# Optimization experiments

Hardware: AMD Instinct MI355X
Metric: run time of the kernel (lower is better)

## Reference

```python
import jax, jax.numpy as jnp
import numpy as np

DMIN, DMAX = -1.0, 1.0
B, I, O, K = 1024, 256, 256, 128

def setup_inputs() -> dict:
    key = jax.random.key(0)
    k1, k2, k3 = jax.random.split(key, 3)
    x = jax.random.normal(k1, (B, I), dtype=jnp.float32)
    bound = 1.0 / np.sqrt(I)
    base_weight = jax.random.uniform(k2, (O, I), dtype=jnp.float32, minval=-bound, maxval=bound)
    coeff = 0.03 * jax.random.normal(k3, (O, I, K), dtype=jnp.float32)
    coeff = coeff - coeff.mean(axis=-1, keepdims=True)
    return {
        'x': x,
        'base_weight': base_weight,
        'spline_coefficients': coeff,
        'spline_scale': jnp.ones((O, I), dtype=jnp.float32),
        'bias': jnp.zeros((O,), dtype=jnp.float32),
    }


def reference(x, base_weight, spline_coefficients, spline_scale, bias):
    num_knots = spline_coefficients.shape[-1]
    step = (DMAX - DMIN) / (num_knots - 1)
    # input activation (tanh) then clamp to spline domain
    p = jnp.tanh(x)                                   # (B, I)
    c = jnp.clip(p, DMIN, DMAX)
    scaled = (c - DMIN) / step                        # in [0, K-1]
    left = jnp.clip(jnp.floor(scaled).astype(jnp.int32), 0, num_knots - 1)
    right = jnp.minimum(left + 1, num_knots - 1)
    frac = scaled - left.astype(p.dtype)              # (B, I)
    # fold spline_scale into coefficients, then gather only the 2 relevant knots
    Cs = spline_coefficients * spline_scale[..., None]  # (O, I, K)
    ii = jnp.arange(x.shape[1])[None, :]                # (1, I) broadcasts with (B, I)
    cl = Cs[:, ii, left]                                # (O, B, I)
    cr = Cs[:, ii, right]                               # (O, B, I)
    spline = jnp.einsum('bi,obi->bo', 1.0 - frac, cl) + jnp.einsum('bi,obi->bo', frac, cr)
    base = jax.nn.silu(p) @ base_weight.T               # (B, O)
    return base + spline + bias[None, :]
```

## Files before the change

### kernel.cpp

```cpp
#include <hip/hip_runtime.h>

constexpr int Bb = 1024;
constexpr int Ii = 256;
constexpr int Oo = 256;
constexpr int Kk = 128;
constexpr int NCH = 8;

typedef unsigned short u16;
typedef u16 ushort4v __attribute__((ext_vector_type(4)));

__device__ __forceinline__ float bf16u_to_f(u16 u) {
    union { unsigned int ui; float f; } c;
    c.ui = ((unsigned int)u) << 16;
    return c.f;
}
__device__ __forceinline__ u16 f_to_bf16(float f) {
    union { float f; unsigned int u; } c; c.f = f;
    unsigned int r = c.u + 0x7fffu + ((c.u >> 16) & 1u);
    return (u16)(r >> 16);
}

__global__ __launch_bounds__(256) void kperm(const float* __restrict__ cs,
                                             const float* __restrict__ scale,
                                             const float* __restrict__ wbase,
                                             u16* __restrict__ cp,
                                             float* __restrict__ wt) {
    __shared__ u16 T[128 * 130];
    int i  = blockIdx.x >> 1;
    int o0 = (blockIdx.x & 1) << 7;
    int t = threadIdx.x;

    {
        int c4 = t & 31;
        int rb = t >> 5;
        const float4* cs4 = (const float4*)cs;
#pragma unroll
        for (int p = 0; p < 16; ++p) {
            int r = p * 8 + rb;
            int o = o0 + r;
            float sc = scale[o * Ii + i];
            float4 val = cs4[(size_t)(o * Ii + i) * (Kk / 4) + c4];
            unsigned int lo = ((unsigned int)f_to_bf16(val.y * sc) << 16) | f_to_bf16(val.x * sc);
            unsigned int hi = ((unsigned int)f_to_bf16(val.w * sc) << 16) | f_to_bf16(val.z * sc);
            *(unsigned int*)&T[r * 130 + c4 * 4]     = lo;
            *(unsigned int*)&T[r * 130 + c4 * 4 + 2] = hi;
        }
    }
    __syncthreads();
    {
        int ol = t & 127;
        int kh = t >> 7;
        u16* dst = cp + ((size_t)i * Kk) * Oo + o0 + ol;
#pragma unroll
        for (int p = 0; p < 64; ++p) {
            int k = p * 2 + kh;
            dst[(size_t)k * Oo] = T[ol * 130 + k];
        }
    }
    if (blockIdx.x < 256) {
        int gid = blockIdx.x * 256 + t;
        wt[gid] = wbase[(gid & 255) * Ii + (gid >> 8)];
    }
}

__global__ __launch_bounds__(256, 4) void kmain(const float* __restrict__ x,
                                                const char* __restrict__ cpb,
                                                const float4* __restrict__ wt4,
                                                float4* __restrict__ part4) {
    __shared__ float4 sf[128];
    int t = threadIdx.x;
    int blk = blockIdx.x;
    int chunk = blk & (NCH - 1);
    int b0 = (blk >> 3) << 2;
    int i0 = chunk << 5;

    if (t < 128) {
        int il = t >> 2, bl = t & 3;
        float xv = x[(size_t)(b0 + bl) * Ii + i0 + il];
        float e2 = __expf(2.f * xv);
        float p = 1.f - 2.f / (e2 + 1.f);
        float s = p / (1.f + __expf(-p));
        float c = fminf(fmaxf(p, -1.f), 1.f);
        float scaled = (c + 1.f) * ((float)(Kk - 1) * 0.5f);
        int l = (int)floorf(scaled);
        l = min(max(l, 0), Kk - 1);
        int rr = min(l + 1, Kk - 1);
        float4 v;
        v.x = scaled - (float)l;
        v.y = s;
        v.z = __int_as_float(l * (Oo * 2));
        v.w = __int_as_float(rr * (Oo * 2));
        sf[t] = v;
    }
    __syncthreads();

    int oq = t & 63;
    int bh = t >> 6;

    float a0 = 0.f, a1 = 0.f, a2 = 0.f, a3 = 0.f;
    const char* cbase = cpb + (size_t)i0 * (Kk * Oo * 2) + oq * 8;
#pragma unroll 8
    for (int il = 0; il < 32; ++il) {
        float4 v = sf[il * 4 + bh];
        float4 w = wt4[(i0 + il) * (Oo / 4) + oq];
        const char* ci = cbase + (size_t)il * (Kk * Oo * 2);
        ushort4v cl = *(const ushort4v*)(ci + __float_as_int(v.z));
        ushort4v cr = *(const ushort4v*)(ci + __float_as_int(v.w));
        float f = v.x, g = 1.f - v.x, s = v.y;
        a0 = fmaf(s, w.x, a0);
        a1 = fmaf(s, w.y, a1);
        a2 = fmaf(s, w.z, a2);
        a3 = fmaf(s, w.w, a3);
        a0 = fmaf(g, bf16u_to_f(cl.x), a0);
        a1 = fmaf(g, bf16u_to_f(cl.y), a1);
        a2 = fmaf(g, bf16u_to_f(cl.z), a2);
        a3 = fmaf(g, bf16u_to_f(cl.w), a3);
        a0 = fmaf(f, bf16u_to_f(cr.x), a0);
        a1 = fmaf(f, bf16u_to_f(cr.y), a1);
        a2 = fmaf(f, bf16u_to_f(cr.z), a2);
        a3 = fmaf(f, bf16u_to_f(cr.w), a3);
    }
    float4 r; r.x = a0; r.y = a1; r.z = a2; r.w = a3;
    part4[(size_t)chunk * (Bb * Oo / 4) + (size_t)(b0 + bh) * (Oo / 4) + oq] = r;
}

__global__ __launch_bounds__(256) void kreduce(const float4* __restrict__ part4,
                                               const float4* __restrict__ bias4,
                                               float4* __restrict__ out4) {
    int gid = blockIdx.x * 256 + threadIdx.x;
    const float4* p = part4 + gid;
    float4 s = p[0];
#pragma unroll
    for (int c = 1; c < NCH; ++c) {
        float4 v = p[(size_t)c * (Bb * Oo / 4)];
        s.x += v.x; s.y += v.y; s.z += v.z; s.w += v.w;
    }
    float4 bv = bias4[gid & 63];
    s.x += bv.x; s.y += bv.y; s.z += bv.z; s.w += bv.w;
    out4[gid] = s;
}

extern "C" void kernel_launch(void* const* d_in, const int* in_sizes, int n_in,
                              void* d_out, int out_size, void* d_ws, size_t ws_size,
                              hipStream_t stream) {
    const float* x     = (const float*)d_in[0];
    const float* wbase = (const float*)d_in[1];
    const float* coeff = (const float*)d_in[2];
    const float* scale = (const float*)d_in[3];
    const float* bias  = (const float*)d_in[4];
    float* out = (float*)d_out;

    char* ws = (char*)d_ws;
    u16*    cp    = (u16*)ws;
    float*  wt    = (float*)(ws + (16u << 20));
    float4* part4 = (float4*)(ws + (17u << 20));

    kperm<<<Ii * 2, 256, 0, stream>>>(coeff, scale, wbase, cp, wt);
    kmain<<<2048, 256, 0, stream>>>(x, (const char*)cp, (const float4*)wt, part4);
    kreduce<<<(Bb * Oo / 4) / 256, 256, 0, stream>>>(part4, (const float4*)bias, (float4*)out);
}
```

Before: 115.8 us.

## Split coefficient permute across more blocks and stage base weights in LDS

The permute kernel is split into four blocks per input (halving both o and k) with a smaller LDS tile. Its global writes become packed 32-bit stores instead of scattered 16-bit stores. The main kernel now stages 8 rows of transposed base weights into shared memory per sub-iteration instead of loading float4 directly from global, and raises occupancy hints to 8 blocks per CU. The staging adds extra barriers per block, and the occupancy hint may pressure registers.

```diff
diff --git a/kernel.cpp b/kernel.cpp
--- a/kernel.cpp
+++ b/kernel.cpp
@@ -7,16 +7,17 @@
 constexpr int NCH = 8;
 
 typedef unsigned short u16;
+typedef unsigned int u32;
 typedef u16 ushort4v __attribute__((ext_vector_type(4)));
 
 __device__ __forceinline__ float bf16u_to_f(u16 u) {
-    union { unsigned int ui; float f; } c;
-    c.ui = ((unsigned int)u) << 16;
+    union { u32 ui; float f; } c;
+    c.ui = ((u32)u) << 16;
     return c.f;
 }
 __device__ __forceinline__ u16 f_to_bf16(float f) {
-    union { float f; unsigned int u; } c; c.f = f;
-    unsigned int r = c.u + 0x7fffu + ((c.u >> 16) & 1u);
+    union { float f; u32 u; } c; c.f = f;
+    u32 r = c.u + 0x7fffu + ((c.u >> 16) & 1u);
     return (u16)(r >> 16);
 }
 
@@ -25,49 +26,54 @@
                                              const float* __restrict__ wbase,
                                              u16* __restrict__ cp,
                                              float* __restrict__ wt) {
-    __shared__ u16 T[128 * 130];
-    int i  = blockIdx.x >> 1;
-    int o0 = (blockIdx.x & 1) << 7;
+    __shared__ u16 T[128 * 66];
+    int blk = blockIdx.x;
+    int i  = blk >> 2;
+    int oh = (blk >> 1) & 1, kh = blk & 1;
+    int o0 = oh << 7, kb = kh << 6;
     int t = threadIdx.x;
 
     {
-        int c4 = t & 31;
-        int rb = t >> 5;
+        int c4 = t & 15;
+        int rb = t >> 4;
         const float4* cs4 = (const float4*)cs;
 #pragma unroll
-        for (int p = 0; p < 16; ++p) {
-            int r = p * 8 + rb;
+        for (int p = 0; p < 8; ++p) {
+            int r = p * 16 + rb;
             int o = o0 + r;
             float sc = scale[o * Ii + i];
-            float4 val = cs4[(size_t)(o * Ii + i) * (Kk / 4) + c4];
-            unsigned int lo = ((unsigned int)f_to_bf16(val.y * sc) << 16) | f_to_bf16(val.x * sc);
-            unsigned int hi = ((unsigned int)f_to_bf16(val.w * sc) << 16) | f_to_bf16(val.z * sc);
-            *(unsigned int*)&T[r * 130 + c4 * 4]     = lo;
-            *(unsigned int*)&T[r * 130 + c4 * 4 + 2] = hi;
+            float4 val = cs4[(size_t)(o * Ii + i) * (Kk / 4) + kh * 16 + c4];
+            int kl = c4 * 4;
+            T[r * 66 + kl + 0] = f_to_bf16(val.x * sc);
+            T[r * 66 + kl + 1] = f_to_bf16(val.y * sc);
+            T[r * 66 + kl + 2] = f_to_bf16(val.z * sc);
+            T[r * 66 + kl + 3] = f_to_bf16(val.w * sc);
         }
     }
     __syncthreads();
     {
-        int ol = t & 127;
-        int kh = t >> 7;
-        u16* dst = cp + ((size_t)i * Kk) * Oo + o0 + ol;
+        int og = t & 63;
+        int kg = t >> 6;
 #pragma unroll
-        for (int p = 0; p < 64; ++p) {
-            int k = p * 2 + kh;
-            dst[(size_t)k * Oo] = T[ol * 130 + k];
+        for (int m = 0; m < 16; ++m) {
+            int kl = kg * 16 + m;
+            u32 lo = T[(og * 2) * 66 + kl];
+            u32 hi = T[(og * 2 + 1) * 66 + kl];
+            *(u32*)&cp[((size_t)i * Kk + kb + kl) * Oo + o0 + og * 2] = lo | (hi << 16);
         }
     }
-    if (blockIdx.x < 256) {
-        int gid = blockIdx.x * 256 + t;
+    if (blk < 256) {
+        int gid = blk * 256 + t;
         wt[gid] = wbase[(gid & 255) * Ii + (gid >> 8)];
     }
 }
 
-__global__ __launch_bounds__(256, 4) void kmain(const float* __restrict__ x,
+__global__ __launch_bounds__(256, 8) void kmain(const float* __restrict__ x,
                                                 const char* __restrict__ cpb,
-                                                const float4* __restrict__ wt4,
+                                                const float* __restrict__ wt,
                                                 float4* __restrict__ part4) {
     __shared__ float4 sf[128];
+    __shared__ float wbuf[8 * 256];
     int t = threadIdx.x;
     int blk = blockIdx.x;
     int chunk = blk & (NCH - 1);
@@ -92,33 +98,45 @@
         v.w = __int_as_float(rr * (Oo * 2));
         sf[t] = v;
     }
-    __syncthreads();
 
     int oq = t & 63;
     int bh = t >> 6;
 
     float a0 = 0.f, a1 = 0.f, a2 = 0.f, a3 = 0.f;
     const char* cbase = cpb + (size_t)i0 * (Kk * Oo * 2) + oq * 8;
-#pragma unroll 8
-    for (int il = 0; il < 32; ++il) {
-        float4 v = sf[il * 4 + bh];
-        float4 w = wt4[(i0 + il) * (Oo / 4) + oq];
-        const char* ci = cbase + (size_t)il * (Kk * Oo * 2);
-        ushort4v cl = *(const ushort4v*)(ci + __float_as_int(v.z));
-        ushort4v cr = *(const ushort4v*)(ci + __float_as_int(v.w));
-        float f = v.x, g = 1.f - v.x, s = v.y;
-        a0 = fmaf(s, w.x, a0);
-        a1 = fmaf(s, w.y, a1);
-        a2 = fmaf(s, w.z, a2);
-        a3 = fmaf(s, w.w, a3);
-        a0 = fmaf(g, bf16u_to_f(cl.x), a0);
-        a1 = fmaf(g, bf16u_to_f(cl.y), a1);
-        a2 = fmaf(g, bf16u_to_f(cl.z), a2);
-        a3 = fmaf(g, bf16u_to_f(cl.w), a3);
-        a0 = fmaf(f, bf16u_to_f(cr.x), a0);
-        a1 = fmaf(f, bf16u_to_f(cr.y), a1);
-        a2 = fmaf(f, bf16u_to_f(cr.z), a2);
-        a3 = fmaf(f, bf16u_to_f(cr.w), a3);
+
+#pragma unroll
+    for (int jb = 0; jb < 4; ++jb) {
+        __syncthreads();
+        {
+            const float* wsrc = wt + (size_t)(i0 + jb * 8) * Oo;
+#pragma unroll
+            for (int p = 0; p < 8; ++p)
+                wbuf[t + p * 256] = wsrc[t + p * 256];
+        }
+        __syncthreads();
+#pragma unroll
+        for (int m = 0; m < 8; ++m) {
+            int il = jb * 8 + m;
+            float4 v = sf[il * 4 + bh];
+            float4 w = *(const float4*)&wbuf[m * 256 + oq * 4];
+            const char* ci = cbase + (size_t)il * (Kk * Oo * 2);
+            ushort4v cl = *(const ushort4v*)(ci + __float_as_int(v.z));
+            ushort4v cr = *(const ushort4v*)(ci + __float_as_int(v.w));
+            float f = v.x, g = 1.f - v.x, s = v.y;
+            a0 = fmaf(s, w.x, a0);
+            a1 = fmaf(s, w.y, a1);
+            a2 = fmaf(s, w.z, a2);
+            a3 = fmaf(s, w.w, a3);
+            a0 = fmaf(g, bf16u_to_f(cl.x), a0);
+            a1 = fmaf(g, bf16u_to_f(cl.y), a1);
+            a2 = fmaf(g, bf16u_to_f(cl.z), a2);
+            a3 = fmaf(g, bf16u_to_f(cl.w), a3);
+            a0 = fmaf(f, bf16u_to_f(cr.x), a0);
+            a1 = fmaf(f, bf16u_to_f(cr.y), a1);
+            a2 = fmaf(f, bf16u_to_f(cr.z), a2);
+            a3 = fmaf(f, bf16u_to_f(cr.w), a3);
+        }
     }
     float4 r; r.x = a0; r.y = a1; r.z = a2; r.w = a3;
     part4[(size_t)chunk * (Bb * Oo / 4) + (size_t)(b0 + bh) * (Oo / 4) + oq] = r;
@@ -155,7 +173,7 @@
     float*  wt    = (float*)(ws + (16u << 20));
     float4* part4 = (float4*)(ws + (17u << 20));
 
-    kperm<<<Ii * 2, 256, 0, stream>>>(coeff, scale, wbase, cp, wt);
-    kmain<<<2048, 256, 0, stream>>>(x, (const char*)cp, (const float4*)wt, part4);
+    kperm<<<1024, 256, 0, stream>>>(coeff, scale, wbase, cp, wt);
+    kmain<<<2048, 256, 0, stream>>>(x, (const char*)cp, wt, part4);
     kreduce<<<(Bb * Oo / 4) / 256, 256, 0, stream>>>(part4, (const float4*)bias, (float4*)out);
 }
```

Measured after the change: 111.0 us. -4.1%, faster.
